# Kernel optimization log

Hardware: AMD Instinct MI355X
Metric: run time of the kernel (lower is better)

The kernel has to match this reference:

```python
import jax, jax.numpy as jnp
import numpy as np

B, S, H, NH, HD = 2, 2048, 2048, 16, 128
MASK_VALUE = -1e10


def setup_inputs() -> dict:
    key = jax.random.key(0)
    ks = jax.random.split(key, 5)
    scale = 1.0 / np.sqrt(H)
    x = jax.random.normal(ks[0], (B, S, H), dtype=jnp.float32)
    Wq = jax.random.normal(ks[1], (H, NH * HD), dtype=jnp.float32) * scale
    Wk = jax.random.normal(ks[2], (H, NH * HD), dtype=jnp.float32) * scale
    Wv = jax.random.normal(ks[3], (H, NH * HD), dtype=jnp.float32) * scale
    Wo = jax.random.normal(ks[4], (NH * HD, H), dtype=jnp.float32) * scale
    # causal boolean mask (B, S, S) as in decoder-style gemma usage
    mask = jnp.broadcast_to(jnp.tril(jnp.ones((S, S), dtype=bool)), (B, S, S))
    return {"x": x, "mask": mask, "Wq": Wq, "Wk": Wk, "Wv": Wv, "Wo": Wo}


def reference(x, mask, Wq, Wk, Wv, Wo):
    b, s, h = x.shape
    # bias-free QKV projections, split into heads -> (b, nh, s, hd)
    def split_heads(y):
        return y.reshape(b, s, NH, HD).transpose(0, 2, 1, 3)
    q = split_heads(x @ Wq)
    k = split_heads(x @ Wk)
    v = split_heads(x @ Wv)
    scores = jnp.einsum('bhtd,bhTd->bhtT', q, k) / jnp.sqrt(jnp.asarray(HD, x.dtype))
    scores = jnp.where(mask[:, None, :, :], scores, MASK_VALUE)
    weights = jax.nn.softmax(scores, axis=-1)
    out = jnp.einsum('bhtT,bhTd->bhtd', weights, v)
    out = out.transpose(0, 2, 1, 3).reshape(b, s, NH * HD)
    return out @ Wo
```

## Files before the change

### kernel.cpp

```cpp
#include <hip/hip_runtime.h>
#include <hip/hip_bf16.h>
#include <stdint.h>

#define DEVFN __device__ __forceinline__

typedef __attribute__((ext_vector_type(8))) short short8;
typedef __attribute__((ext_vector_type(4))) float f32x4;
typedef __attribute__((ext_vector_type(16))) float f32x16;

constexpr int S_LEN = 2048;
constexpr int HDIM  = 2048;
constexpr int NHEAD = 16;
constexpr int HD    = 128;

DEVFN unsigned short f2bf(float f){
  union { float f; unsigned u; } x; x.f = f;
  unsigned r = x.u + 0x7fffu + ((x.u >> 16) & 1u);
  return (unsigned short)(r >> 16);
}

typedef const __attribute__((address_space(1))) void* gas1_ptr;
typedef __attribute__((address_space(3))) void* las3_ptr;

DEVFN void gl_lds16(const void* g, void* l){
  __builtin_amdgcn_global_load_lds((gas1_ptr)g, (las3_ptr)l, 16, 0, 0);
}

DEVFN f32x4 mfma16(short8 a, short8 b, f32x4 c){
  return __builtin_amdgcn_mfma_f32_16x16x32_bf16(a, b, c, 0, 0, 0);
}

DEVFN f32x16 mfma32(short8 a, short8 b, f32x16 c){
  return __builtin_amdgcn_mfma_f32_32x32x16_bf16(a, b, c, 0, 0, 0);
}

DEVFN unsigned cvtpk_bf16(float lo, float hi){
  unsigned w;
  asm("v_cvt_pk_bf16_f32 %0, %1, %2" : "=v"(w) : "v"(lo), "v"(hi));
  return w;
}


__global__ void cast_x_kernel(const float* __restrict__ in, unsigned short* __restrict__ out){
  int i = (blockIdx.x * 256 + threadIdx.x) * 4;
  float4 v = *(const float4*)(in + i);
  ushort4 o;
  o.x = f2bf(v.x); o.y = f2bf(v.y); o.z = f2bf(v.z); o.w = f2bf(v.w);
  *(ushort4*)(out + i) = o;
}

__global__ void transpose_cast_w4(const float* __restrict__ w0, const float* __restrict__ w1,
                                  const float* __restrict__ w2, const float* __restrict__ w3,
                                  unsigned short* __restrict__ out){
  __shared__ float tile[32][33];
  int tx = threadIdx.x, ty = threadIdx.y;
  int kb = blockIdx.x * 32, nb = blockIdx.y * 32, z = blockIdx.z;
  const float* in = (z == 0) ? w0 : (z == 1) ? w1 : (z == 2) ? w2 : w3;
  unsigned short* op = out + (size_t)z * HDIM * HDIM;
  #pragma unroll
  for (int i = 0; i < 4; i++)
    tile[ty + i*8][tx] = in[(size_t)(kb + ty + i*8) * HDIM + nb + tx];
  __syncthreads();
  #pragma unroll
  for (int i = 0; i < 4; i++)
    op[(size_t)(nb + ty + i*8) * HDIM + kb + tx] = f2bf(tile[tx][ty + i*8]);
}


DEVFN void gemm_core_bt(const unsigned short* __restrict__ A,
                        const unsigned short* __restrict__ Bt,
                        int K, int m0, int n0, char* ls, f32x4 (&acc)[4][4]){
  const int t = threadIdx.x;
  const int wid = t >> 6, lane = t & 63;
  const int wr = wid >> 1, wc = wid & 1;
  const int l15 = lane & 15, lg = lane >> 4;
  char* lsA = ls;
  char* lsB = ls + 16384;

  for (int k0 = 0; k0 < K; k0 += 64){
    __syncthreads();
    #pragma unroll
    for (int i = 0; i < 4; i++){
      int o = (t + i*256) * 16;
      int row = o >> 7;
      int col = (o & 127) ^ ((row & 7) << 4);
      gl_lds16((const char*)A + ((size_t)(m0 + row) * K + k0) * 2 + col, lsA + o);
    }
    #pragma unroll
    for (int i = 0; i < 4; i++){
      int o = (t + i*256) * 16;
      int row = o >> 7;
      int col = (o & 127) ^ ((row & 7) << 4);
      gl_lds16((const char*)Bt + ((size_t)(n0 + row) * K + k0) * 2 + col, lsB + o);
    }
    __syncthreads();
    #pragma unroll
    for (int kk = 0; kk < 2; kk++){
      short8 af[4], bfr[4];
      #pragma unroll
      for (int i = 0; i < 4; i++){
        int ra = wr*64 + i*16 + l15;
        af[i]  = *(const short8*)(lsA + ra*128 + ((kk*64 + lg*16) ^ ((ra & 7) << 4)));
        int rb = wc*64 + i*16 + l15;
        bfr[i] = *(const short8*)(lsB + rb*128 + ((kk*64 + lg*16) ^ ((rb & 7) << 4)));
      }
      #pragma unroll
      for (int i = 0; i < 4; i++)
        #pragma unroll
        for (int j = 0; j < 4; j++)
          acc[i][j] = mfma16(af[i], bfr[j], acc[i][j]);
    }
  }
}

__global__ __launch_bounds__(256, 4)
void gemm_qkv(const unsigned short* __restrict__ xb, const unsigned short* __restrict__ Wt,
              unsigned short* __restrict__ Qb, unsigned short* __restrict__ Kb,
              unsigned short* __restrict__ Vt){
  __shared__ __align__(16) char ls[32768];
  f32x4 acc[4][4];
  const f32x4 z4 = {0.f, 0.f, 0.f, 0.f};
  #pragma unroll
  for (int i = 0; i < 4; i++)
    #pragma unroll
    for (int j = 0; j < 4; j++) acc[i][j] = z4;

  const int m0 = blockIdx.x * 128;
  const int n0 = blockIdx.y * 128;
  gemm_core_bt(xb, Wt, HDIM, m0, n0, ls, acc);

  const float qscale = 0.08838834764831845f * 1.4426950408889634f;
  const int t = threadIdx.x, wid = t >> 6, lane = t & 63;
  const int wr = wid >> 1, wc = wid & 1, l15 = lane & 15, lg = lane >> 4;
  const int bb = m0 >> 11, ss0 = m0 & 2047;

  if (n0 < 4096){
    unsigned short* base = (n0 < 2048) ? Qb : Kb;
    const float sc = (n0 < 2048) ? qscale : 1.0f;
    #pragma unroll
    for (int j = 0; j < 4; j++){
      int n = n0 + wc*64 + j*16 + l15;
      int hh = (n >> 7) & 15, d = n & 127;
      #pragma unroll
      for (int i = 0; i < 4; i++){
        #pragma unroll
        for (int r = 0; r < 4; r++){
          int ss = ss0 + wr*64 + i*16 + lg*4 + r;
          base[(((size_t)bb * NHEAD + hh) * S_LEN + ss) * HD + d] = f2bf(acc[i][j][r] * sc);
        }
      }
    }
  } else {
    const int hh = (n0 - 4096) >> 7;
    __syncthreads();
    #pragma unroll
    for (int j = 0; j < 4; j++){
      int nn = wc*64 + j*16 + l15;
      #pragma unroll
      for (int i = 0; i < 4; i++){
        int mmb = (wr*64 + i*16 + lg*4) * 2;
        unsigned w0 = cvtpk_bf16(acc[i][j][0], acc[i][j][1]);
        unsigned w1 = cvtpk_bf16(acc[i][j][2], acc[i][j][3]);
        *(unsigned*)(ls + nn*256 + ((mmb    ) ^ ((nn & 7) << 4))) = w0;
        *(unsigned*)(ls + nn*256 + ((mmb + 4) ^ ((nn & 7) << 4))) = w1;
      }
    }
    __syncthreads();
    unsigned short* vout = Vt + (((size_t)bb * NHEAD + hh) * HD) * S_LEN;
    #pragma unroll
    for (int p = 0; p < 8; p++){
      int idx = p*256 + t;
      int d = idx >> 4;
      int m8 = (idx & 15) * 8;
      short8 v = *(const short8*)(ls + d*256 + ((m8*2) ^ ((d & 7) << 4)));
      *(short8*)(vout + (size_t)d * S_LEN + ss0 + m8) = v;
    }
  }
}

__global__ __launch_bounds__(256, 4)
void gemm_out(const unsigned short* __restrict__ Ob, const unsigned short* __restrict__ Wot,
              float* __restrict__ out){
  __shared__ __align__(16) char ls[32768];
  f32x4 acc[4][4];
  const f32x4 z4 = {0.f, 0.f, 0.f, 0.f};
  #pragma unroll
  for (int i = 0; i < 4; i++)
    #pragma unroll
    for (int j = 0; j < 4; j++) acc[i][j] = z4;

  const int m0 = blockIdx.x * 128;
  const int n0 = blockIdx.y * 128;
  gemm_core_bt(Ob, Wot, HDIM, m0, n0, ls, acc);

  const int t = threadIdx.x, wid = t >> 6, lane = t & 63;
  const int wr = wid >> 1, wc = wid & 1, l15 = lane & 15, lg = lane >> 4;
  #pragma unroll
  for (int i = 0; i < 4; i++){
    #pragma unroll
    for (int r = 0; r < 4; r++){
      int m = m0 + wr*64 + i*16 + lg*4 + r;
      #pragma unroll
      for (int j = 0; j < 4; j++){
        int n = n0 + wc*64 + j*16 + l15;
        out[(size_t)m * HDIM + n] = acc[i][j][r];
      }
    }
  }
}

__global__ __launch_bounds__(256, 2)
void attn_kernel(const unsigned short* __restrict__ Q,
                 const unsigned short* __restrict__ Kg,
                 const unsigned short* __restrict__ Vt,
                 unsigned short* __restrict__ Ob){
  __shared__ __align__(16) unsigned short Kl[2][64*128];
  __shared__ __align__(16) unsigned short Vl[3][128*64];

  const int t = threadIdx.x;
  const int wid = t >> 6, lane = t & 63;
  const int l31 = lane & 31, hi = lane >> 5;
  const int L = blockIdx.x;
  const int bh = L & 31;
  const int z = L >> 5;
  const int qt = (z < 8) ? z : 23 - z;
  const int b = bh >> 4, h = bh & 15;
  const unsigned short* Qp = Q  + (size_t)bh * S_LEN * HD;
  const unsigned short* Kp = Kg + (size_t)bh * S_LEN * HD;
  const unsigned short* Vp = Vt + (size_t)bh * S_LEN * HD;
  const int q0 = qt * 128;
  const int wrow0 = q0 + wid * 32;
  const int qrow = wrow0 + l31;
  const int nt = 2 * qt + 2;
  const int ntw = (wrow0 >> 6) + 1;

  auto stage = [&](int tdx){
    char* kb = (char*)&Kl[tdx & 1][0];
    char* vb = (char*)&Vl[tdx % 3][0];
    const int k0 = tdx * 64;
    #pragma unroll
    for (int i = 0; i < 4; i++){
      int o = (t + i*256) * 16;
      int row = o >> 8;
      int col = (o & 255) ^ ((row & 15) << 4);
      gl_lds16((const char*)(Kp + (size_t)(k0 + row) * HD) + col, kb + o);
    }
    #pragma unroll
    for (int i = 0; i < 4; i++){
      int o = (t + i*256) * 16;
      int row = o >> 7;
      int col = (o & 127) ^ ((row & 7) << 4);
      gl_lds16((const char*)(Vp + (size_t)row * S_LEN + k0) + col, vb + o);
    }
  };

  short8 qf[8];
  #pragma unroll
  for (int dk = 0; dk < 8; dk++)
    qf[dk] = *(const short8*)(Qp + (size_t)qrow * HD + dk*16 + hi*8);

  f32x16 oacc[4];
  #pragma unroll
  for (int db = 0; db < 4; db++)
    #pragma unroll
    for (int r = 0; r < 16; r++) oacc[db][r] = 0.f;
  float mrun = -1e30f, lsum = 0.f;
  short8 paA[4], paB[4];

  auto do_pv = [&](short8 (&pprev)[4], const char* vb){
    __builtin_amdgcn_s_setprio(1);
    #pragma unroll
    for (int ks = 0; ks < 4; ks++){
      #pragma unroll
      for (int db = 0; db < 4; db++){
        int vr = db*32 + l31;
        short8 vf = *(const short8*)(vb + vr*128 + ((ks*32 + hi*16) ^ ((vr & 7) << 4)));
        oacc[db] = mfma32(vf, pprev[ks], oacc[db]);
      }
    }
    __builtin_amdgcn_s_setprio(0);
  };

  auto body = [&](int tdx, short8 (&pcur)[4], short8 (&pprev)[4]){
    if (tdx + 1 < nt) stage(tdx + 1);
    const char* Kb_ = (const char*)&Kl[tdx & 1][0];
    const bool doQK = (tdx < ntw);
    const bool doPV = (tdx >= 1) && (tdx <= ntw);

    f32x16 sacc[2];
    if (doQK){
      #pragma unroll
      for (int cb = 0; cb < 2; cb++)
        #pragma unroll
        for (int r = 0; r < 16; r++) sacc[cb][r] = 0.f;
      __builtin_amdgcn_s_setprio(1);
      #pragma unroll
      for (int dk = 0; dk < 8; dk++){
        #pragma unroll
        for (int cb = 0; cb < 2; cb++){
          int kr = cb*32 + l31;
          short8 af = *(const short8*)(Kb_ + kr*256 + ((dk*32 + hi*16) ^ ((kr & 15) << 4)));
          sacc[cb] = mfma32(af, qf[dk], sacc[cb]);
        }
      }
      __builtin_amdgcn_s_setprio(0);
    }

    if (doPV) do_pv(pprev, (const char*)&Vl[(tdx - 1) % 3][0]);

    if (doQK){
      const int k0 = tdx * 64;
      if (tdx == ntw - 1){
        #pragma unroll
        for (int cb = 0; cb < 2; cb++)
          #pragma unroll
          for (int r = 0; r < 16; r++){
            int kcol = k0 + cb*32 + (r & 3) + 8*(r >> 2) + 4*hi;
            if (kcol > qrow) sacc[cb][r] = -1e30f;
          }
      }
      float mv[8];
      #pragma unroll
      for (int i = 0; i < 8; i++)
        mv[i] = fmaxf(fmaxf(sacc[0][i], sacc[0][i+8]), fmaxf(sacc[1][i], sacc[1][i+8]));
      #pragma unroll
      for (int s = 4; s > 0; s >>= 1)
        #pragma unroll
        for (int i = 0; i < 4; i++)
          if (i < s) mv[i] = fmaxf(mv[i], mv[i+s]);
      float mx = fmaxf(mv[0], __shfl_xor(mv[0], 32, 64));
      if (!__all(mx <= mrun + 8.f)){
        float mnew = fmaxf(mrun, mx);
        float alpha = exp2f(mrun - mnew);
        mrun = mnew;
        lsum *= alpha;
        #pragma unroll
        for (int db = 0; db < 4; db++)
          #pragma unroll
          for (int r = 0; r < 16; r++) oacc[db][r] *= alpha;
      }
      float ls = 0.f;
      #pragma unroll
      for (int cb = 0; cb < 2; cb++)
        #pragma unroll
        for (int r = 0; r < 16; r++){
          float p = exp2f(sacc[cb][r] - mrun);
          sacc[cb][r] = p;
          ls += p;
        }
      lsum += ls;
      #pragma unroll
      for (int ks = 0; ks < 4; ks++){
        int cb = ks >> 1, bs = (ks & 1) * 8;
        unsigned B1 = cvtpk_bf16(sacc[cb][bs+0], sacc[cb][bs+1]);
        unsigned B2 = cvtpk_bf16(sacc[cb][bs+2], sacc[cb][bs+3]);
        unsigned A1 = cvtpk_bf16(sacc[cb][bs+4], sacc[cb][bs+5]);
        unsigned A2 = cvtpk_bf16(sacc[cb][bs+6], sacc[cb][bs+7]);
        asm("v_permlane32_swap_b32 %0, %1" : "+v"(B1), "+v"(A1));
        asm("v_permlane32_swap_b32 %0, %1" : "+v"(B2), "+v"(A2));
        union { unsigned u[4]; short8 v; } pk;
        pk.u[0] = B1; pk.u[1] = B2; pk.u[2] = A1; pk.u[3] = A2;
        pcur[ks] = pk.v;
      }
    }

    asm volatile("s_waitcnt vmcnt(0)" ::: "memory");
    __builtin_amdgcn_s_barrier();
  };

  stage(0);
  asm volatile("s_waitcnt vmcnt(0)" ::: "memory");
  __builtin_amdgcn_s_barrier();

  #pragma unroll 1
  for (int tt = 0; tt < nt; tt += 2){
    body(tt,     paA, paB);
    body(tt + 1, paB, paA);
  }
  if (ntw == nt) do_pv(paB, (const char*)&Vl[(nt - 1) % 3][0]);

  float lt = lsum + __shfl_xor(lsum, 32, 64);
  float inv = 1.f / lt;
  #pragma unroll
  for (int db = 0; db < 4; db++)
    #pragma unroll
    for (int r = 0; r < 16; r++) oacc[db][r] *= inv;

  __builtin_amdgcn_s_barrier();
  char* reg_lds = (char*)&Kl[0][0] + wid * 8192;
  #pragma unroll
  for (int ms = 0; ms < 8; ms++){
    int db = ms >> 1, bs = (ms & 1) * 8;
    unsigned B1 = cvtpk_bf16(oacc[db][bs+0], oacc[db][bs+1]);
    unsigned B2 = cvtpk_bf16(oacc[db][bs+2], oacc[db][bs+3]);
    unsigned A1 = cvtpk_bf16(oacc[db][bs+4], oacc[db][bs+5]);
    unsigned A2 = cvtpk_bf16(oacc[db][bs+6], oacc[db][bs+7]);
    asm("v_permlane32_swap_b32 %0, %1" : "+v"(B1), "+v"(A1));
    asm("v_permlane32_swap_b32 %0, %1" : "+v"(B2), "+v"(A2));
    union { unsigned u[4]; short8 v; } pk;
    pk.u[0] = B1; pk.u[1] = B2; pk.u[2] = A1; pk.u[3] = A2;
    int byteo = l31*256 + ((ms*32 + hi*16) ^ ((l31 & 7) << 4));
    *(short8*)(reg_lds + byteo) = pk.v;
  }
  #pragma unroll
  for (int i = 0; i < 8; i++){
    int r = (lane >> 4) + i*4;
    int c = lane & 15;
    short8 v = *(const short8*)(reg_lds + r*256 + ((c*16) ^ ((r & 7) << 4)));
    *(short8*)(Ob + ((size_t)(b * S_LEN + wrow0 + r)) * 2048 + h*128 + c*8) = v;
  }
}

extern "C" void kernel_launch(void* const* d_in, const int* in_sizes, int n_in,
                              void* d_out, int out_size, void* d_ws, size_t ws_size,
                              hipStream_t stream){
  const float* x  = (const float*)d_in[0];
  const float* Wq = (const float*)d_in[2];
  const float* Wk = (const float*)d_in[3];
  const float* Wv = (const float*)d_in[4];
  const float* Wo = (const float*)d_in[5];

  char* ws = (char*)d_ws;
  unsigned short* xb  = (unsigned short*)(ws);
  unsigned short* Wt  = (unsigned short*)(ws + 16777216);
  unsigned short* Wot = (unsigned short*)(ws + 41943040);
  unsigned short* Qb  = (unsigned short*)(ws + 50331648);
  unsigned short* Kb  = (unsigned short*)(ws + 67108864);
  unsigned short* Vt  = (unsigned short*)(ws + 83886080);
  unsigned short* Ob  = xb;

  dim3 tb(32, 8);
  cast_x_kernel<<<8192, 256, 0, stream>>>(x, xb);
  transpose_cast_w4<<<dim3(64, 64, 4), tb, 0, stream>>>(Wq, Wk, Wv, Wo, Wt);

  gemm_qkv<<<dim3(32, 48), 256, 0, stream>>>(xb, Wt, Qb, Kb, Vt);

  attn_kernel<<<512, 256, 0, stream>>>(Qb, Kb, Vt, Ob);

  gemm_out<<<dim3(32, 16), 256, 0, stream>>>(Ob, Wot, (float*)d_out);
}
```

Before: 231.8 us.

## Triple-buffer GEMM LDS pipeline with 256x128 tiles and XCD-aware block mapping

Replaces the synchronous load-then-compute GEMM core with a triple-buffered LDS pipeline. Global-to-LDS copies for tile k+2 are issued in chunks between MFMA phases, coordinated with explicit waitcnt, barriers and setprio. Blocks grow to 512 threads covering 256x128 output tiles, and block indices are remapped so each XCD works on contiguous M rows for better L2 reuse. The goal is to hide global memory latency and cut per-iteration sync stalls, at the cost of about 144KB of LDS per block, which limits occupancy to one block per CU, plus more intricate manual scheduling.

```diff
diff --git a/kernel.cpp b/kernel.cpp
--- a/kernel.cpp
+++ b/kernel.cpp
@@ -66,58 +66,126 @@
     op[(size_t)(nb + ty + i*8) * HDIM + kb + tx] = f2bf(tile[tx][ty + i*8]);
 }
 
-
-DEVFN void gemm_core_bt(const unsigned short* __restrict__ A,
+DEVFN void gemm_core_p4(const unsigned short* __restrict__ A,
                         const unsigned short* __restrict__ Bt,
                         int K, int m0, int n0, char* ls, f32x4 (&acc)[4][4]){
-  const int t = threadIdx.x;
-  const int wid = t >> 6, lane = t & 63;
-  const int wr = wid >> 1, wc = wid & 1;
+  const int tid = threadIdx.x;
+  const int wid = tid >> 6, lane = tid & 63;
+  const int wm = wid >> 1, wn = wid & 1;
   const int l15 = lane & 15, lg = lane >> 4;
-  char* lsA = ls;
-  char* lsB = ls + 16384;
-
-  for (int k0 = 0; k0 < K; k0 += 64){
-    __syncthreads();
-    #pragma unroll
-    for (int i = 0; i < 4; i++){
-      int o = (t + i*256) * 16;
-      int row = o >> 7;
-      int col = (o & 127) ^ ((row & 7) << 4);
-      gl_lds16((const char*)A + ((size_t)(m0 + row) * K + k0) * 2 + col, lsA + o);
-    }
-    #pragma unroll
-    for (int i = 0; i < 4; i++){
-      int o = (t + i*256) * 16;
-      int row = o >> 7;
-      int col = (o & 127) ^ ((row & 7) << 4);
-      gl_lds16((const char*)Bt + ((size_t)(n0 + row) * K + k0) * 2 + col, lsB + o);
-    }
-    __syncthreads();
-    #pragma unroll
-    for (int kk = 0; kk < 2; kk++){
-      short8 af[4], bfr[4];
-      #pragma unroll
-      for (int i = 0; i < 4; i++){
-        int ra = wr*64 + i*16 + l15;
-        af[i]  = *(const short8*)(lsA + ra*128 + ((kk*64 + lg*16) ^ ((ra & 7) << 4)));
-        int rb = wc*64 + i*16 + l15;
-        bfr[i] = *(const short8*)(lsB + rb*128 + ((kk*64 + lg*16) ^ ((rb & 7) << 4)));
-      }
-      #pragma unroll
-      for (int i = 0; i < 4; i++)
-        #pragma unroll
-        for (int j = 0; j < 4; j++)
-          acc[i][j] = mfma16(af[i], bfr[j], acc[i][j]);
-    }
+  const int nt = K >> 6;
+
+  auto stage_chunk = [&](int buf, int kt, int c){
+    char* lb = ls + buf * 49152;
+    if (c < 2){
+      #pragma unroll
+      for (int i = 0; i < 2; i++){
+        int o = (tid + (c*2 + i)*512) * 16;
+        int row = o >> 7;
+        int col = (o & 127) ^ ((row & 7) << 4);
+        gl_lds16((const char*)A + ((size_t)(m0 + row) * K + kt*64) * 2 + col, lb + o);
+      }
+    } else {
+      #pragma unroll
+      for (int i = 0; i < 2; i++){
+        int o = (tid + i*512) * 16;
+        int row = o >> 7;
+        int col = (o & 127) ^ ((row & 7) << 4);
+        gl_lds16((const char*)Bt + ((size_t)(n0 + row) * K + kt*64) * 2 + col, lb + 32768 + o);
+      }
+    }
+  };
+
+  #pragma unroll
+  for (int c = 0; c < 3; c++) stage_chunk(0, 0, c);
+  #pragma unroll
+  for (int c = 0; c < 3; c++) stage_chunk(1, 1, c);
+  asm volatile("s_waitcnt vmcnt(6)" ::: "memory");
+  __builtin_amdgcn_s_barrier();
+
+  int rb = 0;
+  #pragma unroll 1
+  for (int kt = 0; kt < nt; kt++){
+    char* lb  = ls + rb * 49152;
+    char* lbB = lb + 32768;
+    const int wbuf = (rb + 2 >= 3) ? rb - 1 : rb + 2;
+    const bool pre = (kt + 2 < nt);
+
+    auto rdA = [&](int i, int kk) -> short8 {
+      int ra = wm*64 + i*16 + l15;
+      return *(const short8*)(lb + ra*128 + ((kk*64 + lg*16) ^ ((ra & 7) << 4)));
+    };
+    auto rdB = [&](int j, int kk) -> short8 {
+      int rr = wn*64 + j*16 + l15;
+      return *(const short8*)(lbB + rr*128 + ((kk*64 + lg*16) ^ ((rr & 7) << 4)));
+    };
+
+    short8 a0, a1, a2, a3, b0, b1, b2, b3;
+
+    a0 = rdA(0,0); a1 = rdA(1,0);
+    b0 = rdB(0,0); b1 = rdB(1,0); b2 = rdB(2,0); b3 = rdB(3,0);
+    if (pre) stage_chunk(wbuf, kt + 2, 0);
+    __builtin_amdgcn_s_barrier();
+    asm volatile("s_waitcnt lgkmcnt(0)" ::: "memory");
+    __builtin_amdgcn_sched_barrier(0);
+    __builtin_amdgcn_s_setprio(1);
+    acc[0][0] = mfma16(a0, b0, acc[0][0]); acc[1][0] = mfma16(a1, b0, acc[1][0]);
+    acc[0][1] = mfma16(a0, b1, acc[0][1]); acc[1][1] = mfma16(a1, b1, acc[1][1]);
+    acc[0][2] = mfma16(a0, b2, acc[0][2]); acc[1][2] = mfma16(a1, b2, acc[1][2]);
+    acc[0][3] = mfma16(a0, b3, acc[0][3]); acc[1][3] = mfma16(a1, b3, acc[1][3]);
+    __builtin_amdgcn_s_setprio(0);
+    __builtin_amdgcn_s_barrier();
+
+    a2 = rdA(2,0); a3 = rdA(3,0);
+    if (pre) stage_chunk(wbuf, kt + 2, 1);
+    __builtin_amdgcn_s_barrier();
+    asm volatile("s_waitcnt lgkmcnt(0)" ::: "memory");
+    __builtin_amdgcn_sched_barrier(0);
+    __builtin_amdgcn_s_setprio(1);
+    acc[2][0] = mfma16(a2, b0, acc[2][0]); acc[3][0] = mfma16(a3, b0, acc[3][0]);
+    acc[2][1] = mfma16(a2, b1, acc[2][1]); acc[3][1] = mfma16(a3, b1, acc[3][1]);
+    acc[2][2] = mfma16(a2, b2, acc[2][2]); acc[3][2] = mfma16(a3, b2, acc[3][2]);
+    acc[2][3] = mfma16(a2, b3, acc[2][3]); acc[3][3] = mfma16(a3, b3, acc[3][3]);
+    __builtin_amdgcn_s_setprio(0);
+    __builtin_amdgcn_s_barrier();
+
+    a0 = rdA(0,1); a1 = rdA(1,1);
+    b0 = rdB(0,1); b1 = rdB(1,1); b2 = rdB(2,1); b3 = rdB(3,1);
+    if (pre) stage_chunk(wbuf, kt + 2, 2);
+    __builtin_amdgcn_s_barrier();
+    asm volatile("s_waitcnt lgkmcnt(0)" ::: "memory");
+    __builtin_amdgcn_sched_barrier(0);
+    __builtin_amdgcn_s_setprio(1);
+    acc[0][0] = mfma16(a0, b0, acc[0][0]); acc[1][0] = mfma16(a1, b0, acc[1][0]);
+    acc[0][1] = mfma16(a0, b1, acc[0][1]); acc[1][1] = mfma16(a1, b1, acc[1][1]);
+    acc[0][2] = mfma16(a0, b2, acc[0][2]); acc[1][2] = mfma16(a1, b2, acc[1][2]);
+    acc[0][3] = mfma16(a0, b3, acc[0][3]); acc[1][3] = mfma16(a1, b3, acc[1][3]);
+    __builtin_amdgcn_s_setprio(0);
+    __builtin_amdgcn_s_barrier();
+
+    a2 = rdA(2,1); a3 = rdA(3,1);
+    if (pre)               asm volatile("s_waitcnt vmcnt(6)" ::: "memory");
+    else if (kt + 1 < nt)  asm volatile("s_waitcnt vmcnt(0)" ::: "memory");
+    __builtin_amdgcn_s_barrier();
+    asm volatile("s_waitcnt lgkmcnt(0)" ::: "memory");
+    __builtin_amdgcn_sched_barrier(0);
+    __builtin_amdgcn_s_setprio(1);
+    acc[2][0] = mfma16(a2, b0, acc[2][0]); acc[3][0] = mfma16(a3, b0, acc[3][0]);
+    acc[2][1] = mfma16(a2, b1, acc[2][1]); acc[3][1] = mfma16(a3, b1, acc[3][1]);
+    acc[2][2] = mfma16(a2, b2, acc[2][2]); acc[3][2] = mfma16(a3, b2, acc[3][2]);
+    acc[2][3] = mfma16(a2, b3, acc[2][3]); acc[3][3] = mfma16(a3, b3, acc[3][3]);
+    __builtin_amdgcn_s_setprio(0);
+    __builtin_amdgcn_s_barrier();
+
+    rb = (rb + 1 == 3) ? 0 : rb + 1;
   }
 }
 
-__global__ __launch_bounds__(256, 4)
+__global__ __launch_bounds__(512, 2)
 void gemm_qkv(const unsigned short* __restrict__ xb, const unsigned short* __restrict__ Wt,
               unsigned short* __restrict__ Qb, unsigned short* __restrict__ Kb,
               unsigned short* __restrict__ Vt){
-  __shared__ __align__(16) char ls[32768];
+  __shared__ __align__(16) char ls[147456];
   f32x4 acc[4][4];
   const f32x4 z4 = {0.f, 0.f, 0.f, 0.f};
   #pragma unroll
@@ -125,13 +193,15 @@
     #pragma unroll
     for (int j = 0; j < 4; j++) acc[i][j] = z4;
 
-  const int m0 = blockIdx.x * 128;
-  const int n0 = blockIdx.y * 128;
-  gemm_core_bt(xb, Wt, HDIM, m0, n0, ls, acc);
+  const int xcd = blockIdx.x & 7, idx = blockIdx.x >> 3;
+  const int m0 = (xcd * 2 + idx / 48) * 256;
+  const int n0 = (idx % 48) * 128;
+
+  gemm_core_p4(xb, Wt, HDIM, m0, n0, ls, acc);
 
   const float qscale = 0.08838834764831845f * 1.4426950408889634f;
-  const int t = threadIdx.x, wid = t >> 6, lane = t & 63;
-  const int wr = wid >> 1, wc = wid & 1, l15 = lane & 15, lg = lane >> 4;
+  const int tid = threadIdx.x, wid = tid >> 6, lane = tid & 63;
+  const int wm = wid >> 1, wn = wid & 1, l15 = lane & 15, lg = lane >> 4;
   const int bb = m0 >> 11, ss0 = m0 & 2047;
 
   if (n0 < 4096){
@@ -139,13 +209,13 @@
     const float sc = (n0 < 2048) ? qscale : 1.0f;
     #pragma unroll
     for (int j = 0; j < 4; j++){
-      int n = n0 + wc*64 + j*16 + l15;
+      int n = n0 + wn*64 + j*16 + l15;
       int hh = (n >> 7) & 15, d = n & 127;
       #pragma unroll
       for (int i = 0; i < 4; i++){
         #pragma unroll
         for (int r = 0; r < 4; r++){
-          int ss = ss0 + wr*64 + i*16 + lg*4 + r;
+          int ss = ss0 + wm*64 + i*16 + lg*4 + r;
           base[(((size_t)bb * NHEAD + hh) * S_LEN + ss) * HD + d] = f2bf(acc[i][j][r] * sc);
         }
       }
@@ -155,33 +225,33 @@
     __syncthreads();
     #pragma unroll
     for (int j = 0; j < 4; j++){
-      int nn = wc*64 + j*16 + l15;
+      int nn = wn*64 + j*16 + l15;
       #pragma unroll
       for (int i = 0; i < 4; i++){
-        int mmb = (wr*64 + i*16 + lg*4) * 2;
+        int mmb = (wm*64 + i*16 + lg*4) * 2;
         unsigned w0 = cvtpk_bf16(acc[i][j][0], acc[i][j][1]);
         unsigned w1 = cvtpk_bf16(acc[i][j][2], acc[i][j][3]);
-        *(unsigned*)(ls + nn*256 + ((mmb    ) ^ ((nn & 7) << 4))) = w0;
-        *(unsigned*)(ls + nn*256 + ((mmb + 4) ^ ((nn & 7) << 4))) = w1;
+        *(unsigned*)(ls + nn*512 + ((mmb    ) ^ ((nn & 7) << 4))) = w0;
+        *(unsigned*)(ls + nn*512 + ((mmb + 4) ^ ((nn & 7) << 4))) = w1;
       }
     }
     __syncthreads();
     unsigned short* vout = Vt + (((size_t)bb * NHEAD + hh) * HD) * S_LEN;
     #pragma unroll
     for (int p = 0; p < 8; p++){
-      int idx = p*256 + t;
-      int d = idx >> 4;
-      int m8 = (idx & 15) * 8;
-      short8 v = *(const short8*)(ls + d*256 + ((m8*2) ^ ((d & 7) << 4)));
-      *(short8*)(vout + (size_t)d * S_LEN + ss0 + m8) = v;
+      int idx2 = p*512 + tid;
+      int d = idx2 >> 5;
+      int ck = idx2 & 31;
+      short8 v = *(const short8*)(ls + d*512 + ((ck*16) ^ ((d & 7) << 4)));
+      *(short8*)(vout + (size_t)d * S_LEN + ss0 + ck*8) = v;
     }
   }
 }
 
-__global__ __launch_bounds__(256, 4)
+__global__ __launch_bounds__(512, 2)
 void gemm_out(const unsigned short* __restrict__ Ob, const unsigned short* __restrict__ Wot,
               float* __restrict__ out){
-  __shared__ __align__(16) char ls[32768];
+  __shared__ __align__(16) char ls[147456];
   f32x4 acc[4][4];
   const f32x4 z4 = {0.f, 0.f, 0.f, 0.f};
   #pragma unroll
@@ -189,20 +259,22 @@
     #pragma unroll
     for (int j = 0; j < 4; j++) acc[i][j] = z4;
 
-  const int m0 = blockIdx.x * 128;
-  const int n0 = blockIdx.y * 128;
-  gemm_core_bt(Ob, Wot, HDIM, m0, n0, ls, acc);
-
-  const int t = threadIdx.x, wid = t >> 6, lane = t & 63;
-  const int wr = wid >> 1, wc = wid & 1, l15 = lane & 15, lg = lane >> 4;
+  const int xcd = blockIdx.x & 7, idx = blockIdx.x >> 3;
+  const int m0 = (xcd * 2 + idx / 16) * 256;
+  const int n0 = (idx % 16) * 128;
+
+  gemm_core_p4(Ob, Wot, HDIM, m0, n0, ls, acc);
+
+  const int tid = threadIdx.x, wid = tid >> 6, lane = tid & 63;
+  const int wm = wid >> 1, wn = wid & 1, l15 = lane & 15, lg = lane >> 4;
   #pragma unroll
   for (int i = 0; i < 4; i++){
     #pragma unroll
     for (int r = 0; r < 4; r++){
-      int m = m0 + wr*64 + i*16 + lg*4 + r;
+      int m = m0 + wm*64 + i*16 + lg*4 + r;
       #pragma unroll
       for (int j = 0; j < 4; j++){
-        int n = n0 + wc*64 + j*16 + l15;
+        int n = n0 + wn*64 + j*16 + l15;
         out[(size_t)m * HDIM + n] = acc[i][j][r];
       }
     }
@@ -433,9 +505,9 @@
   cast_x_kernel<<<8192, 256, 0, stream>>>(x, xb);
   transpose_cast_w4<<<dim3(64, 64, 4), tb, 0, stream>>>(Wq, Wk, Wv, Wo, Wt);
 
-  gemm_qkv<<<dim3(32, 48), 256, 0, stream>>>(xb, Wt, Qb, Kb, Vt);
+  gemm_qkv<<<768, 512, 0, stream>>>(xb, Wt, Qb, Kb, Vt);
 
   attn_kernel<<<512, 256, 0, stream>>>(Qb, Kb, Vt, Ob);
 
-  gemm_out<<<dim3(32, 16), 256, 0, stream>>>(Ob, Wot, (float*)d_out);
-}
+  gemm_out<<<256, 512, 0, stream>>>(Ob, Wot, (float*)d_out);
+}
```

Result: slower. 244.9 us (+5.7%).
